# Kernel tuning notes

Measured on AMD Instinct MI355X. Metric: run time of the kernel, lower is better.

The kernel has to match this reference:

```python
import jax, jax.numpy as jnp
import numpy as np

NUM_SLOTS = 128
HIDDEN_DIM = 4096
EMA_ALPHA = 0.1
WRITE_TOP_K = 2048
T_TOKENS = 8192
K_RET = 4
BATCH_IDX = 0


def setup_inputs() -> dict:
    key = jax.random.key(0)
    k1, k2, k3, k4, k5 = jax.random.split(key, 5)
    hidden_states = jax.random.normal(k1, (T_TOKENS, HIDDEN_DIM), dtype=jnp.float32)
    # attention weights over K retrieved slots: normalized to a distribution per token
    raw = jax.random.uniform(k2, (T_TOKENS, K_RET), dtype=jnp.float32)
    attention_weights = raw / raw.sum(axis=-1, keepdims=True)
    slot_indices = jax.random.randint(k3, (T_TOKENS, K_RET), 0, NUM_SLOTS)
    memory = jax.random.normal(k4, (1, NUM_SLOTS, HIDDEN_DIM), dtype=jnp.float32)
    W_imp = jax.random.normal(k5, (1, HIDDEN_DIM), dtype=jnp.float32) * 0.02
    b_imp = jnp.zeros((1,), dtype=jnp.float32)
    return {
        "hidden_states": hidden_states,
        "attention_weights": attention_weights,
        "slot_indices": slot_indices,
        "memory": memory,
        "W_imp": W_imp,
        "b_imp": b_imp,
    }


def _compute_importance(hidden_states, attention_weights, W_imp, b_imp):
    # magnitude: ||h_t||_2, [T]
    magnitude = jnp.linalg.norm(hidden_states, axis=-1)
    # attention surprise: normalized entropy over K slots, [T]
    attn = attention_weights
    entropy = -(attn * jnp.log(attn + 1e-8)).sum(axis=-1)
    max_entropy = jnp.log(jnp.asarray(attn.shape[-1], dtype=jnp.float32))
    surprise = entropy / jnp.maximum(max_entropy, 1e-8)
    importance = magnitude * (1.0 + surprise)  # 'combined' mode
    learned_score = hidden_states @ W_imp[0] + b_imp[0]  # [T]
    return importance + jax.nn.sigmoid(learned_score)


def reference(hidden_states, attention_weights, slot_indices, memory, W_imp, b_imp):
    # importance-based top-K token selection
    importance = _compute_importance(hidden_states, attention_weights, W_imp, b_imp)
    _, topk_idx = jax.lax.top_k(importance, WRITE_TOP_K)
    h_sel = hidden_states[topk_idx]          # [Ksel, D]
    si_sel = slot_indices[topk_idx]          # [Ksel, K]

    # membership[t, n] = 1 if slot n appears anywhere in token t's retrieved slots
    # (matches torch's (slot_indices == idx).any(dim=-1))
    onehot = jax.nn.one_hot(si_sel, NUM_SLOTS, dtype=jnp.float32)  # [Ksel, K, N]
    member = (onehot.sum(axis=1) > 0).astype(jnp.float32)          # [Ksel, N]

    counts = member.sum(axis=0)                                    # [N]
    sums = jnp.einsum("tn,td->nd", member, h_sel)                  # [N, D]
    agg = sums / jnp.maximum(counts, 1.0)[:, None]                 # segment mean

    current = memory[BATCH_IDX]                                    # [N, D]
    updated = EMA_ALPHA * agg + (1.0 - EMA_ALPHA) * current
    new_slots = jnp.where(counts[:, None] > 0, updated, current)
    return memory.at[BATCH_IDX].set(new_slots)
```

## Files before the change

kernel.cpp:

```cpp
#include <hip/hip_runtime.h>
#include <math.h>

#define T_TOK 8192
#define HDIM 4096
#define NSLOT 128
#define KRET 4
#define TOPK 2048
#define ALPHA 0.1f
#define MAXC 2048

__global__ __launch_bounds__(256) void importance_kernel(
    const float* __restrict__ h, const float* __restrict__ attn,
    const float* __restrict__ W, const float* __restrict__ b,
    float* __restrict__ imp)
{
    const int wid  = threadIdx.x >> 6;
    const int lane = threadIdx.x & 63;
    const int t = blockIdx.x * 4 + wid;
    const float4* hv = reinterpret_cast<const float4*>(h + (size_t)t * HDIM);
    const float4* Wv = reinterpret_cast<const float4*>(W);
    float sumsq = 0.f, dot = 0.f;
    #pragma unroll 4
    for (int i = 0; i < 16; i++) {
        float4 x = hv[lane + i * 64];
        float4 w = Wv[lane + i * 64];
        sumsq += x.x * x.x + x.y * x.y + x.z * x.z + x.w * x.w;
        dot   += x.x * w.x + x.y * w.y + x.z * w.z + x.w * w.w;
    }
    #pragma unroll
    for (int off = 32; off > 0; off >>= 1) {
        sumsq += __shfl_down(sumsq, off);
        dot   += __shfl_down(dot, off);
    }
    if (lane == 0) {
        float mag = sqrtf(sumsq);
        float ent = 0.f;
        #pragma unroll
        for (int k = 0; k < KRET; k++) {
            float a = attn[t * KRET + k];
            ent -= a * logf(a + 1e-8f);
        }
        float surprise = ent / logf(4.0f);
        float score = dot + b[0];
        float sig = 1.0f / (1.0f + expf(-score));
        imp[t] = mag * (1.0f + surprise) + sig;
    }
}

__global__ __launch_bounds__(256) void selectlist_kernel(
    const float* __restrict__ imp, const int* __restrict__ si,
    int* __restrict__ lists, int* __restrict__ counts)
{
    const int slot = blockIdx.x;
    const int tid  = threadIdx.x;
    __shared__ unsigned s_u[T_TOK];
    __shared__ int s_hist[256];
    __shared__ int s_scan[256];
    __shared__ unsigned s_prefix;
    __shared__ int s_want;

    for (int i = tid; i < T_TOK; i += 256)
        s_u[i] = __float_as_uint(imp[i]);
    if (tid == 0) { s_prefix = 0u; s_want = TOPK; }
    __syncthreads();

    for (int pass = 0; pass < 4; pass++) {
        const int p = 24 - pass * 8;
        const unsigned himask = (pass == 0) ? 0u : (0xFFFFFFFFu << (p + 8));
        const unsigned pref = s_prefix;
        const int want = s_want;
        s_hist[tid] = 0;
        __syncthreads();
        for (int j = tid; j < T_TOK; j += 256) {
            unsigned u = s_u[j];
            if ((u & himask) == pref) atomicAdd(&s_hist[(u >> p) & 255], 1);
        }
        __syncthreads();
        s_scan[tid] = s_hist[tid];
        __syncthreads();
        for (int off = 1; off < 256; off <<= 1) {
            int add = (tid + off < 256) ? s_scan[tid + off] : 0;
            __syncthreads();
            s_scan[tid] += add;
            __syncthreads();
        }
        int sufb  = s_scan[tid];
        int sufb1 = (tid < 255) ? s_scan[tid + 1] : 0;
        if (sufb >= want && sufb1 < want) {
            s_prefix = pref | ((unsigned)tid << p);
            s_want = want - sufb1;
        }
        __syncthreads();
    }
    const unsigned thr = s_prefix;
    const int ties_allowed = s_want;

    const int base = tid * 32;
    int eqcnt = 0;
    #pragma unroll 8
    for (int j = 0; j < 32; j++) eqcnt += (s_u[base + j] == thr);
    __syncthreads();
    s_scan[tid] = eqcnt;
    __syncthreads();
    for (int off = 1; off < 256; off <<= 1) {
        int v = s_scan[tid];
        int add = (tid >= off) ? s_scan[tid - off] : 0;
        __syncthreads();
        s_scan[tid] = v + add;
        __syncthreads();
    }
    const int tie_base = s_scan[tid] - eqcnt;

    const int4* si4 = reinterpret_cast<const int4*>(si);
    unsigned mask = 0;
    int local = 0;
    int trun = tie_base;
    #pragma unroll 8
    for (int j = 0; j < 32; j++) {
        const int t = base + j;
        unsigned u = s_u[t];
        bool sel = (u > thr) || (u == thr && trun < ties_allowed);
        if (u == thr) trun++;
        int4 s = si4[t];
        bool mem = (s.x == slot) | (s.y == slot) | (s.z == slot) | (s.w == slot);
        if (sel && mem) { mask |= (1u << j); local++; }
    }
    __syncthreads();
    s_scan[tid] = local;
    __syncthreads();
    for (int off = 1; off < 256; off <<= 1) {
        int v = s_scan[tid];
        int add = (tid >= off) ? s_scan[tid - off] : 0;
        __syncthreads();
        s_scan[tid] = v + add;
        __syncthreads();
    }
    int pos = s_scan[tid] - local;
    int* mylist = lists + (size_t)slot * MAXC;
    for (int j = 0; j < 32; j++) {
        if (mask & (1u << j)) mylist[pos++] = base + j;
    }
    if (tid == 255) counts[slot] = s_scan[255];
}

__global__ __launch_bounds__(256) void update_kernel(
    const float* __restrict__ h, const float* __restrict__ mem,
    const int* __restrict__ lists, const int* __restrict__ counts,
    float* __restrict__ out)
{
    const int slot = blockIdx.x >> 2;
    const int chunk = blockIdx.x & 3;
    const int cnt = counts[slot];
    __shared__ int s_list[MAXC];
    for (int i = threadIdx.x; i < cnt; i += 256)
        s_list[i] = lists[(size_t)slot * MAXC + i];
    __syncthreads();

    const int dbase = chunk * 1024 + threadIdx.x * 4;
    float4 acc = make_float4(0.f, 0.f, 0.f, 0.f);
    int i = 0;
    for (; i + 4 <= cnt; i += 4) {
        int t0 = s_list[i], t1 = s_list[i + 1];
        int t2 = s_list[i + 2], t3 = s_list[i + 3];
        float4 x0 = *reinterpret_cast<const float4*>(h + (size_t)t0 * HDIM + dbase);
        float4 x1 = *reinterpret_cast<const float4*>(h + (size_t)t1 * HDIM + dbase);
        float4 x2 = *reinterpret_cast<const float4*>(h + (size_t)t2 * HDIM + dbase);
        float4 x3 = *reinterpret_cast<const float4*>(h + (size_t)t3 * HDIM + dbase);
        acc.x += x0.x + x1.x + x2.x + x3.x;
        acc.y += x0.y + x1.y + x2.y + x3.y;
        acc.z += x0.z + x1.z + x2.z + x3.z;
        acc.w += x0.w + x1.w + x2.w + x3.w;
    }
    for (; i < cnt; i++) {
        int t0 = s_list[i];
        float4 x0 = *reinterpret_cast<const float4*>(h + (size_t)t0 * HDIM + dbase);
        acc.x += x0.x; acc.y += x0.y; acc.z += x0.z; acc.w += x0.w;
    }

    const size_t o = (size_t)slot * HDIM + dbase;
    float4 cur = *reinterpret_cast<const float4*>(mem + o);
    float4 r;
    if (cnt > 0) {
        float inv = 1.0f / (float)cnt;
        r.x = ALPHA * (acc.x * inv) + (1.f - ALPHA) * cur.x;
        r.y = ALPHA * (acc.y * inv) + (1.f - ALPHA) * cur.y;
        r.z = ALPHA * (acc.z * inv) + (1.f - ALPHA) * cur.z;
        r.w = ALPHA * (acc.w * inv) + (1.f - ALPHA) * cur.w;
    } else {
        r = cur;
    }
    *reinterpret_cast<float4*>(out + o) = r;
}

extern "C" void kernel_launch(void* const* d_in, const int* in_sizes, int n_in,
                              void* d_out, int out_size, void* d_ws, size_t ws_size,
                              hipStream_t stream) {
    const float* h    = (const float*)d_in[0];
    const float* attn = (const float*)d_in[1];
    const int*   si   = (const int*)d_in[2];
    const float* mem  = (const float*)d_in[3];
    const float* W    = (const float*)d_in[4];
    const float* b    = (const float*)d_in[5];
    float* out = (float*)d_out;

    char* ws = (char*)d_ws;
    float* imp    = (float*)(ws);
    int*   counts = (int*)(ws + 65536);
    int*   lists  = (int*)(ws + 131072);

    importance_kernel<<<T_TOK / 4, 256, 0, stream>>>(h, attn, W, b, imp);
    selectlist_kernel<<<NSLOT, 256, 0, stream>>>(imp, si, lists, counts);
    update_kernel<<<NSLOT * 4, 256, 0, stream>>>(h, mem, lists, counts, out);
}
```

Baseline: 64.96 us.

## Compute top-k threshold once and build slot lists inside update kernel

The radix-select threshold was recomputed redundantly by each of the 128 slot blocks. Now a single block computes it once and writes a per-token selection bitmask. The per-slot membership list is built inside the update kernel with wave ballots, which removes the global list/count round trip. The trade-off is that the threshold runs on only one block (serial), and every update block (4 per slot) rescans all 8192 slot-index entries, using 32KB of LDS for the lists.

```diff
diff --git a/kernel.cpp b/kernel.cpp
--- a/kernel.cpp
+++ b/kernel.cpp
@@ -7,7 +7,6 @@
 #define KRET 4
 #define TOPK 2048
 #define ALPHA 0.1f
-#define MAXC 2048
 
 __global__ __launch_bounds__(256) void importance_kernel(
     const float* __restrict__ h, const float* __restrict__ attn,
@@ -47,12 +46,10 @@
     }
 }
 
-__global__ __launch_bounds__(256) void selectlist_kernel(
-    const float* __restrict__ imp, const int* __restrict__ si,
-    int* __restrict__ lists, int* __restrict__ counts)
+__global__ __launch_bounds__(256) void threshold_kernel(
+    const float* __restrict__ imp, unsigned* __restrict__ selbits)
 {
-    const int slot = blockIdx.x;
-    const int tid  = threadIdx.x;
+    const int tid = threadIdx.x;
     __shared__ unsigned s_u[T_TOK];
     __shared__ int s_hist[256];
     __shared__ int s_scan[256];
@@ -109,72 +106,78 @@
         s_scan[tid] = v + add;
         __syncthreads();
     }
-    const int tie_base = s_scan[tid] - eqcnt;
-
-    const int4* si4 = reinterpret_cast<const int4*>(si);
-    unsigned mask = 0;
-    int local = 0;
-    int trun = tie_base;
+    int trun = s_scan[tid] - eqcnt;
+
+    unsigned bits = 0u;
     #pragma unroll 8
     for (int j = 0; j < 32; j++) {
-        const int t = base + j;
-        unsigned u = s_u[t];
+        unsigned u = s_u[base + j];
         bool sel = (u > thr) || (u == thr && trun < ties_allowed);
         if (u == thr) trun++;
-        int4 s = si4[t];
-        bool mem = (s.x == slot) | (s.y == slot) | (s.z == slot) | (s.w == slot);
-        if (sel && mem) { mask |= (1u << j); local++; }
-    }
-    __syncthreads();
-    s_scan[tid] = local;
-    __syncthreads();
-    for (int off = 1; off < 256; off <<= 1) {
-        int v = s_scan[tid];
-        int add = (tid >= off) ? s_scan[tid - off] : 0;
-        __syncthreads();
-        s_scan[tid] = v + add;
-        __syncthreads();
-    }
-    int pos = s_scan[tid] - local;
-    int* mylist = lists + (size_t)slot * MAXC;
-    for (int j = 0; j < 32; j++) {
-        if (mask & (1u << j)) mylist[pos++] = base + j;
-    }
-    if (tid == 255) counts[slot] = s_scan[255];
-}
-
-__global__ __launch_bounds__(256) void update_kernel(
-    const float* __restrict__ h, const float* __restrict__ mem,
-    const int* __restrict__ lists, const int* __restrict__ counts,
+        bits |= (sel ? 1u : 0u) << j;
+    }
+    selbits[tid] = bits;
+}
+
+__global__ __launch_bounds__(256) void update_fused_kernel(
+    const float* __restrict__ h, const int* __restrict__ si,
+    const float* __restrict__ mem, const unsigned* __restrict__ selbits,
     float* __restrict__ out)
 {
     const int slot = blockIdx.x >> 2;
     const int chunk = blockIdx.x & 3;
-    const int cnt = counts[slot];
-    __shared__ int s_list[MAXC];
-    for (int i = threadIdx.x; i < cnt; i += 256)
-        s_list[i] = lists[(size_t)slot * MAXC + i];
-    __syncthreads();
-
-    const int dbase = chunk * 1024 + threadIdx.x * 4;
+    const int tid = threadIdx.x;
+    const int w = tid >> 6, lane = tid & 63;
+
+    __shared__ unsigned s_bits[256];
+    __shared__ int s_list[4][2048];
+    __shared__ int s_wcnt[4];
+
+    s_bits[tid] = selbits[tid];
+    __syncthreads();
+
+    const int4* si4 = reinterpret_cast<const int4*>(si);
+    int base = 0;
+    for (int it = 0; it < 32; it++) {
+        const int t = (w << 11) + (it << 6) + lane;
+        bool sel = (s_bits[t >> 5] >> (t & 31)) & 1u;
+        int4 s = si4[t];
+        bool mem4 = (s.x == slot) | (s.y == slot) | (s.z == slot) | (s.w == slot);
+        bool m = sel && mem4;
+        unsigned long long bal = __ballot(m);
+        if (m) {
+            int pos = base + (int)__popcll(bal & ((1ull << lane) - 1ull));
+            s_list[w][pos] = t;
+        }
+        base += (int)__popcll(bal);
+    }
+    if (lane == 0) s_wcnt[w] = base;
+    __syncthreads();
+
+    const int cnt = s_wcnt[0] + s_wcnt[1] + s_wcnt[2] + s_wcnt[3];
+    const int dbase = chunk * 1024 + tid * 4;
     float4 acc = make_float4(0.f, 0.f, 0.f, 0.f);
-    int i = 0;
-    for (; i + 4 <= cnt; i += 4) {
-        int t0 = s_list[i], t1 = s_list[i + 1];
-        int t2 = s_list[i + 2], t3 = s_list[i + 3];
-        float4 x0 = *reinterpret_cast<const float4*>(h + (size_t)t0 * HDIM + dbase);
-        float4 x1 = *reinterpret_cast<const float4*>(h + (size_t)t1 * HDIM + dbase);
-        float4 x2 = *reinterpret_cast<const float4*>(h + (size_t)t2 * HDIM + dbase);
-        float4 x3 = *reinterpret_cast<const float4*>(h + (size_t)t3 * HDIM + dbase);
-        acc.x += x0.x + x1.x + x2.x + x3.x;
-        acc.y += x0.y + x1.y + x2.y + x3.y;
-        acc.z += x0.z + x1.z + x2.z + x3.z;
-        acc.w += x0.w + x1.w + x2.w + x3.w;
-    }
-    for (; i < cnt; i++) {
-        int t0 = s_list[i];
-        float4 x0 = *reinterpret_cast<const float4*>(h + (size_t)t0 * HDIM + dbase);
-        acc.x += x0.x; acc.y += x0.y; acc.z += x0.z; acc.w += x0.w;
+    for (int wv = 0; wv < 4; wv++) {
+        const int n = s_wcnt[wv];
+        const int* lst = s_list[wv];
+        int i = 0;
+        for (; i + 4 <= n; i += 4) {
+            int t0 = lst[i], t1 = lst[i + 1];
+            int t2 = lst[i + 2], t3 = lst[i + 3];
+            float4 x0 = *reinterpret_cast<const float4*>(h + (size_t)t0 * HDIM + dbase);
+            float4 x1 = *reinterpret_cast<const float4*>(h + (size_t)t1 * HDIM + dbase);
+            float4 x2 = *reinterpret_cast<const float4*>(h + (size_t)t2 * HDIM + dbase);
+            float4 x3 = *reinterpret_cast<const float4*>(h + (size_t)t3 * HDIM + dbase);
+            acc.x += x0.x + x1.x + x2.x + x3.x;
+            acc.y += x0.y + x1.y + x2.y + x3.y;
+            acc.z += x0.z + x1.z + x2.z + x3.z;
+            acc.w += x0.w + x1.w + x2.w + x3.w;
+        }
+        for (; i < n; i++) {
+            int t0 = lst[i];
+            float4 x0 = *reinterpret_cast<const float4*>(h + (size_t)t0 * HDIM + dbase);
+            acc.x += x0.x; acc.y += x0.y; acc.z += x0.z; acc.w += x0.w;
+        }
     }
 
     const size_t o = (size_t)slot * HDIM + dbase;
@@ -204,11 +207,10 @@
     float* out = (float*)d_out;
 
     char* ws = (char*)d_ws;
-    float* imp    = (float*)(ws);
-    int*   counts = (int*)(ws + 65536);
-    int*   lists  = (int*)(ws + 131072);
+    float*    imp     = (float*)(ws);
+    unsigned* selbits = (unsigned*)(ws + 65536);
 
     importance_kernel<<<T_TOK / 4, 256, 0, stream>>>(h, attn, W, b, imp);
-    selectlist_kernel<<<NSLOT, 256, 0, stream>>>(imp, si, lists, counts);
-    update_kernel<<<NSLOT * 4, 256, 0, stream>>>(h, mem, lists, counts, out);
-}
+    threshold_kernel<<<1, 256, 0, stream>>>(imp, selbits);
+    update_fused_kernel<<<NSLOT * 4, 256, 0, stream>>>(h, si, mem, selbits, out);
+}
```

New measurement: 71.73 us. 10.4% more time.
